# Kernel tuning notes

Hardware: AMD Instinct MI355X
Metric: run time of the kernel (lower is better)

The kernel has to match this reference:

```python
import jax, jax.numpy as jnp
import numpy as np

D = 3            # pseudo-coordinate dimensionality
KS = 5           # kernel size per dim (open B-spline, degree 1)
K = KS ** D      # 125 kernel weight slices
S = 2 ** D       # 8 active linear-basis corners per edge
_COMBOS = np.array([[(s >> d) & 1 for d in range(D)] for s in range(S)], dtype=np.int32)  # [S, D]
_STRIDES = np.array([KS ** (D - 1 - d) for d in range(D)], dtype=np.int32)                # [D]


def spline_basis(pseudo):
    """Degree-1 open B-spline tensor-product basis. pseudo: [E, D] in [0,1].
    Returns basis weights [E, S] and flat kernel indices [E, S]."""
    pos = pseudo * (KS - 1)
    i0 = jnp.clip(jnp.floor(pos), 0, KS - 2).astype(jnp.int32)     # [E, D]
    frac = pos - i0                                                 # [E, D]
    combos = jnp.asarray(_COMBOS)                                   # [S, D]
    basis = jnp.prod(jnp.where(combos[None] == 1, frac[:, None, :], 1.0 - frac[:, None, :]), axis=-1)  # [E, S]
    idx = jnp.sum((i0[:, None, :] + combos[None]) * jnp.asarray(_STRIDES)[None, None, :], axis=-1)      # [E, S]
    return basis, idx


def spline_conv(x, row, col, basis, idx, W, b):
    """out[i] = 1/|N(i)| * sum_{j in N(i)} sum_s b_s(u_ij) * x[j] @ W[k_s] + b.
    x: [N, Fin], W: [K, Fin, Fout]."""
    N = x.shape[0]
    Fout = W.shape[2]
    z = jnp.einsum('ni,kio->nko', x, W).reshape(N * K, Fout)        # [N*K, Fout]
    gathered = z[col[:, None] * K + idx]                            # [E, S, Fout]
    msg = jnp.einsum('es,eso->eo', basis, gathered)                 # [E, Fout]
    out = jax.ops.segment_sum(msg, row, num_segments=N)
    deg = jax.ops.segment_sum(jnp.ones_like(msg[:, 0]), row, num_segments=N)
    return out / jnp.maximum(deg, 1.0)[:, None] + b


def setup_inputs():
    key = jax.random.key(0)
    ks = jax.random.split(key, 13)
    N, E, Fin, Fout = 20000, 320000, 32, 32

    def u(k, shape, size):
        bound = 1.0 / np.sqrt(size)
        return jax.random.uniform(k, shape, jnp.float32, -bound, bound)

    return dict(
        x=jax.random.normal(ks[0], (N, Fin), jnp.float32),
        edge_index=jax.random.randint(ks[1], (2, E), 0, N, dtype=jnp.int32),
        pseudo=jax.random.uniform(ks[2], (E, D), jnp.float32),
        stn1_w=u(ks[3], (K, 1, 64), 1 * S), stn1_b=u(ks[4], (64,), 1 * S),
        stn2_w=u(ks[5], (K, 64, 64), 64 * S), stn2_b=u(ks[6], (64,), 64 * S),
        stn3_w=u(ks[7], (64, 64), 64), stn3_b=u(ks[8], (64,), 64),
        stn4_w=u(ks[9], (64, 3), 64), stn4_b=u(ks[10], (3,), 64),
        conv_w=u(ks[11], (K, Fin, Fout), Fin * S), conv_b=u(ks[12], (Fout,), Fin * S),
    )


def reference(x, edge_index, pseudo, stn1_w, stn1_b, stn2_w, stn2_b,
              stn3_w, stn3_b, stn4_w, stn4_b, conv_w, conv_b):
    N = x.shape[0]
    row, col = edge_index[0], edge_index[1]
    basis, idx = spline_basis(pseudo)
    # local spatial-transformer path: SplineConv(1->64) -> SplineConv(64->64) -> Linear(64->64) -> Linear(64->3)
    h = jnp.ones((N, 1), x.dtype)
    h = jax.nn.elu(spline_conv(h, row, col, basis, idx, stn1_w, stn1_b))
    h = jax.nn.elu(spline_conv(h, row, col, basis, idx, stn2_w, stn2_b))
    h = jax.nn.elu(h @ stn3_w + stn3_b)
    t = h @ stn4_w + stn4_b                                          # [N, 3] per-node pseudo-coord offset
    new_pseudo = jnp.clip(pseudo + t[col] - t[row], 0.0, 1.0)        # transformed pseudo-coordinates
    basis2, idx2 = spline_basis(new_pseudo)
    return spline_conv(x, row, col, basis2, idx2, conv_w, conv_b)
```

## Files before the change

kernel.cpp:

```cpp
#include <hip/hip_runtime.h>
#include <hip/hip_bf16.h>
#include <math.h>


typedef short  s16x8 __attribute__((ext_vector_type(8)));
typedef float  f32x4 __attribute__((ext_vector_type(4)));
typedef _Float16 h16x2 __attribute__((ext_vector_type(2)));

__device__ __forceinline__ unsigned short f2b(float f) {
    __hip_bfloat16 h = __float2bfloat16(f);
    return __builtin_bit_cast(unsigned short, h);
}
__device__ __forceinline__ unsigned short f2h(float f) {
    _Float16 h = (_Float16)f;
    return __builtin_bit_cast(unsigned short, h);
}
__device__ __forceinline__ float h2f(unsigned short u) {
    _Float16 h = __builtin_bit_cast(_Float16, u);
    return (float)h;
}
__device__ __forceinline__ unsigned int fdup(float f) {
    unsigned int h = f2h(f);
    return h | (h << 16);
}
__device__ __forceinline__ h16x2 u2h2(unsigned int u) {
    return __builtin_bit_cast(h16x2, u);
}

__device__ __forceinline__ void spline8(const float u0, const float u1, const float u2,
                                        float* __restrict__ b, int* __restrict__ id) {
    const float u[3] = {u0, u1, u2};
    const int strides[3] = {25, 5, 1};
    float fr[3];
    int   i0[3];
#pragma unroll
    for (int d = 0; d < 3; ++d) {
        float p = u[d] * 4.0f;
        float f = floorf(p);
        f = fminf(fmaxf(f, 0.0f), 3.0f);
        i0[d] = (int)f;
        fr[d] = p - f;
    }
#pragma unroll
    for (int s = 0; s < 8; ++s) {
        float bb = 1.0f;
        int   ii = 0;
#pragma unroll
        for (int d = 0; d < 3; ++d) {
            int c = (s >> d) & 1;
            bb *= c ? fr[d] : (1.0f - fr[d]);
            ii += (i0[d] + c) * strides[d];
        }
        b[s] = bb;
        id[s] = ii;
    }
}

__global__ void hist_kernel(const int* __restrict__ row, const int* __restrict__ col,
                            int* __restrict__ histR, int* __restrict__ histC, int E) {
    int e = blockIdx.x * blockDim.x + threadIdx.x;
    if (e >= E) return;
    atomicAdd(&histR[row[e]], 1);
    atomicAdd(&histC[col[e]], 1);
}

__global__ __launch_bounds__(1024) void scan2_kernel(
        const int* __restrict__ histC, const int* __restrict__ histR,
        int* __restrict__ cstart, int* __restrict__ cursorC,
        int* __restrict__ rowStart, int* __restrict__ cursorR, int N) {
    __shared__ int wsX[16], wsY[16];
    __shared__ int carX, carY;
    int t = threadIdx.x, lane = t & 63, w = t >> 6;
    if (t == 0) { carX = 0; carY = 0; }
    __syncthreads();
    for (int base = 0; base < N; base += 1024) {
        int i = base + t;
        int vx = (i < N) ? histC[i] : 0;
        int vy = (i < N) ? histR[i] : 0;
        int sx = vx, sy = vy;
#pragma unroll
        for (int off = 1; off < 64; off <<= 1) {
            int ux = __shfl_up(sx, off);
            int uy = __shfl_up(sy, off);
            if (lane >= off) { sx += ux; sy += uy; }
        }
        if (lane == 63) { wsX[w] = sx; wsY[w] = sy; }
        __syncthreads();
        if (w == 0 && lane < 16) {
            int ax = wsX[lane], ay = wsY[lane];
#pragma unroll
            for (int off = 1; off < 16; off <<= 1) {
                int ux = __shfl_up(ax, off);
                int uy = __shfl_up(ay, off);
                if (lane >= off) { ax += ux; ay += uy; }
            }
            wsX[lane] = ax; wsY[lane] = ay;
        }
        __syncthreads();
        int wx = (w > 0 ? wsX[w - 1] : 0) + carX;
        int wy = (w > 0 ? wsY[w - 1] : 0) + carY;
        if (i < N) {
            int ex = wx + sx - vx;
            int ey = wy + sy - vy;
            cstart[i] = ex; cursorC[i] = ex;
            rowStart[i] = ey; cursorR[i] = ey;
        }
        __syncthreads();
        if (t == 0) { carX += wsX[15]; carY += wsY[15]; }
        __syncthreads();
    }
}

__global__ void scatterbasis_kernel(
        const int* __restrict__ row, const int* __restrict__ col,
        const float* __restrict__ pseudo,
        int* __restrict__ cursorC, int* __restrict__ cursorR,
        int* __restrict__ jpos, int* __restrict__ colS, int* __restrict__ rs,
        unsigned int* __restrict__ basisH, unsigned char* __restrict__ idxb,
        float* __restrict__ basisR, unsigned char* __restrict__ idxR, int E) {
    int e = blockIdx.x * blockDim.x + threadIdx.x;
    if (e >= E) return;
    int c = col[e], r = row[e];
    int jc = atomicAdd(&cursorC[c], 1);
    int jr = atomicAdd(&cursorR[r], 1);
    jpos[e] = jc;
    colS[jc] = c;
    rs[jc] = jr;
    float b[8]; int id[8];
    spline8(pseudo[e * 3 + 0], pseudo[e * 3 + 1], pseudo[e * 3 + 2], b, id);
#pragma unroll
    for (int s = 0; s < 8; ++s) {
        basisH[(size_t)jc * 8 + s] = fdup(b[s]);
        idxb[(size_t)jc * 8 + s] = (unsigned char)id[s];
        basisR[(size_t)jr * 8 + s] = b[s];
        idxR[(size_t)jr * 8 + s] = (unsigned char)id[s];
    }
}

__global__ void basis1_kernel(const float* __restrict__ pseudo, const int* __restrict__ jpos,
                              float* __restrict__ basis, unsigned char* __restrict__ idxb, int E) {
    int e = blockIdx.x * blockDim.x + threadIdx.x;
    if (e >= E) return;
    float b[8]; int id[8];
    spline8(pseudo[e * 3 + 0], pseudo[e * 3 + 1], pseudo[e * 3 + 2], b, id);
    int j = jpos ? jpos[e] : e;
#pragma unroll
    for (int s = 0; s < 8; ++s) { basis[(size_t)j * 8 + s] = b[s]; idxb[(size_t)j * 8 + s] = (unsigned char)id[s]; }
}

__global__ void basis2h_kernel(const float* __restrict__ pseudo, const float* __restrict__ t,
                               const int* __restrict__ row, const int* __restrict__ col,
                               const int* __restrict__ jpos,
                               unsigned int* __restrict__ basisH,
                               unsigned char* __restrict__ idxb, int E) {
    int e = blockIdx.x * blockDim.x + threadIdx.x;
    if (e >= E) return;
    int r = row[e], c = col[e];
    float u[3];
#pragma unroll
    for (int d = 0; d < 3; ++d) {
        float v = pseudo[e * 3 + d] + t[c * 3 + d] - t[r * 3 + d];
        u[d] = fminf(fmaxf(v, 0.0f), 1.0f);
    }
    float b[8]; int id[8];
    spline8(u[0], u[1], u[2], b, id);
    int j = jpos[e];
#pragma unroll
    for (int s = 0; s < 8; ++s) { basisH[(size_t)j * 8 + s] = fdup(b[s]); idxb[(size_t)j * 8 + s] = (unsigned char)id[s]; }
}

__global__ void basis2_kernel(const float* __restrict__ pseudo, const float* __restrict__ t,
                              const int* __restrict__ row, const int* __restrict__ col,
                              float* __restrict__ basis, unsigned char* __restrict__ idxb, int E) {
    int e = blockIdx.x * blockDim.x + threadIdx.x;
    if (e >= E) return;
    int r = row[e], c = col[e];
    float u[3];
#pragma unroll
    for (int d = 0; d < 3; ++d) {
        float v = pseudo[e * 3 + d] + t[c * 3 + d] - t[r * 3 + d];
        u[d] = fminf(fmaxf(v, 0.0f), 1.0f);
    }
    float b[8]; int id[8];
    spline8(u[0], u[1], u[2], b, id);
#pragma unroll
    for (int s = 0; s < 8; ++s) { basis[(size_t)e * 8 + s] = b[s]; idxb[(size_t)e * 8 + s] = (unsigned char)id[s]; }
}

__global__ void castbf_kernel(const float* __restrict__ in, unsigned short* __restrict__ out,
                              int n) {
    int t = blockIdx.x * blockDim.x + threadIdx.x;
    if (t < n) out[t] = f2b(in[t]);
}

__global__ void pack_w_kernel(const float* __restrict__ W, unsigned short* __restrict__ BF,
                              int Kc, int Fin, int Fout, int ksteps, int CH) {
    int t = blockIdx.x * blockDim.x + threadIdx.x;
    int total = Kc * Fout * Fin;
    if (t >= total) return;
    int c = t / Fin;
    int i = t % Fin;
    int kk = c / Fout, o = c % Fout;
    int split = o / CH;
    int cp = split * (Kc * CH) + kk * CH + (o % CH);
    int ct = cp >> 4, lr = cp & 15;
    int step = i >> 5, rem = i & 31, lg = rem >> 3, jj = rem & 7;
    size_t dst = ((((size_t)ct * ksteps + step) * 4 + lg) * 16 + lr) * 8 + jj;
    BF[dst] = f2b(W[((size_t)kk * Fin + i) * Fout + o]);
}

__global__ __launch_bounds__(256) void phaseB1s_kernel(
        const float* __restrict__ W1, const float* __restrict__ basisR,
        const unsigned char* __restrict__ idxR, const int* __restrict__ rowStart,
        const int* __restrict__ histR, const float* __restrict__ b1,
        unsigned short* __restrict__ h1b, int N) {
    __shared__ float w[125 * 64];
    for (int i = threadIdx.x; i < 125 * 64; i += 256) w[i] = W1[i];
    __syncthreads();
    int n = blockIdx.x * 4 + (threadIdx.x >> 6);
    if (n >= N) return;
    int l = threadIdx.x & 63;
    int s0 = rowStart[n], cnt = histR[n];
    float a = 0.0f;
    for (int i = 0; i < cnt; ++i) {
        const float4* bp = (const float4*)(basisR + (size_t)(s0 + i) * 8);
        float4 b0 = bp[0], b1v = bp[1];
        const uchar4* ip = (const uchar4*)(idxR + (size_t)(s0 + i) * 8);
        uchar4 i0 = ip[0], i1 = ip[1];
        a += b0.x * w[i0.x * 64 + l] + b0.y * w[i0.y * 64 + l]
           + b0.z * w[i0.z * 64 + l] + b0.w * w[i0.w * 64 + l]
           + b1v.x * w[i1.x * 64 + l] + b1v.y * w[i1.y * 64 + l]
           + b1v.z * w[i1.z * 64 + l] + b1v.w * w[i1.w * 64 + l];
    }
    float v = a / fmaxf((float)cnt, 1.0f) + b1[l];
    v = (v > 0.0f) ? v : (expf(v) - 1.0f);
    h1b[(size_t)n * 64 + l] = f2b(v);
}

template<int KSTEPS, int SPLITS, int NODES>
__global__ __launch_bounds__(512) void fusedconv_kernel(
        const unsigned short* __restrict__ A,
        const unsigned short* __restrict__ BF,
        const unsigned int* __restrict__ basisH, const unsigned char* __restrict__ idxb,
        const int* __restrict__ cstart, const int* __restrict__ colS,
        const int* __restrict__ rs,
        unsigned short* __restrict__ msgP, int N, int E) {
    const int ZLD = 2008;
    __shared__ unsigned short ztile[NODES * 2008];
    int n0 = blockIdx.x * NODES;
    if (n0 >= N) return;
    int w = threadIdx.x >> 6, l = threadIdx.x & 63;
    int lr = l & 15, lg = l >> 4;
    const int KD = KSTEPS * 32;
    int arow = n0 + lr; if (arow > N - 1) arow = N - 1;
    s16x8 a[KSTEPS];
#pragma unroll
    for (int st = 0; st < KSTEPS; ++st)
        a[st] = *(const s16x8*)(A + (size_t)arow * KD + st * 32 + lg * 8);
    int estart = cstart[n0];
    int eend = (n0 + NODES < N) ? cstart[n0 + NODES] : E;
    int g = threadIdx.x >> 3, chp = threadIdx.x & 7;
    for (int s = 0; s < SPLITS; ++s) {
        for (int ct = w; ct < 125; ct += 8) {
            f32x4 acc = (f32x4){0.f, 0.f, 0.f, 0.f};
#pragma unroll
            for (int st = 0; st < KSTEPS; ++st) {
                const unsigned short* bp =
                    BF + ((((size_t)(s * 125 + ct) * KSTEPS + st) * 4 + lg) * 16 + lr) * 8;
                s16x8 b = *(const s16x8*)bp;
                acc = __builtin_amdgcn_mfma_f32_16x16x32_bf16(a[st], b, acc, 0, 0, 0);
            }
#pragma unroll
            for (int r = 0; r < 4; ++r) {
                int rl = lg * 4 + r;
                if (rl < NODES)
                    ztile[rl * ZLD + ct * 16 + lr] = f2h(acc[r]);
            }
        }
        __syncthreads();
        unsigned int* mp = (unsigned int*)(msgP + (size_t)s * E * 16);
        for (int j = estart + g; j < eend; j += 64) {
            int node = colS[j] - n0;
            const uint4* bhp = (const uint4*)(basisH + (size_t)j * 8);
            uint4 bA = bhp[0], bB = bhp[1];
            const uchar4* ip = (const uchar4*)(idxb + (size_t)j * 8);
            uchar4 i0 = ip[0], i1 = ip[1];
            const unsigned int* zr = (const unsigned int*)(ztile + node * ZLD);
            unsigned int v0 = zr[i0.x * 8 + chp];
            unsigned int v1 = zr[i0.y * 8 + chp];
            unsigned int v2 = zr[i0.z * 8 + chp];
            unsigned int v3 = zr[i0.w * 8 + chp];
            unsigned int v4 = zr[i1.x * 8 + chp];
            unsigned int v5 = zr[i1.y * 8 + chp];
            unsigned int v6 = zr[i1.z * 8 + chp];
            unsigned int v7 = zr[i1.w * 8 + chp];
            h16x2 ta = u2h2(bA.x) * u2h2(v0);
            ta = u2h2(bA.y) * u2h2(v1) + ta;
            ta = u2h2(bA.z) * u2h2(v2) + ta;
            ta = u2h2(bA.w) * u2h2(v3) + ta;
            h16x2 tb = u2h2(bB.x) * u2h2(v4);
            tb = u2h2(bB.y) * u2h2(v5) + tb;
            tb = u2h2(bB.z) * u2h2(v6) + tb;
            tb = u2h2(bB.w) * u2h2(v7) + tb;
            h16x2 m = ta + tb;
            mp[(size_t)rs[j] * 8 + chp] = __builtin_bit_cast(unsigned int, m);
        }
        __syncthreads();
    }
}

__global__ __launch_bounds__(256) void phaseBs2stn_kernel(
        const unsigned short* __restrict__ msgP, const int* __restrict__ rowStart,
        const int* __restrict__ histR, const float* __restrict__ b2,
        const float* __restrict__ w3, const float* __restrict__ b3,
        const float* __restrict__ w4, const float* __restrict__ b4,
        float* __restrict__ tt, int N, int E) {
    __shared__ float sh[4][64];
    __shared__ float sh3[4][64];
    int wid = threadIdx.x >> 6, l = threadIdx.x & 63;
    int n = blockIdx.x * 4 + wid;
    if (n >= N) return;
    int s0 = rowStart[n], cnt = histR[n];
    const unsigned short* mp = msgP + (size_t)(l >> 4) * E * 16 + (l & 15);
    float a = 0.0f;
    for (int i = 0; i < cnt; ++i)
        a += h2f(mp[(size_t)(s0 + i) * 16]);
    float v = a / fmaxf((float)cnt, 1.0f) + b2[l];
    v = (v > 0.0f) ? v : (expf(v) - 1.0f);
    sh[wid][l] = v;
    __builtin_amdgcn_wave_barrier();
    float v3 = b3[l];
#pragma unroll
    for (int i = 0; i < 64; ++i) v3 += sh[wid][i] * w3[i * 64 + l];
    v3 = (v3 > 0.0f) ? v3 : (expf(v3) - 1.0f);
    sh3[wid][l] = v3;
    __builtin_amdgcn_wave_barrier();
    if (l < 3) {
        float tv = b4[l];
#pragma unroll
        for (int i = 0; i < 64; ++i) tv += sh3[wid][i] * w4[i * 3 + l];
        tt[(size_t)n * 3 + l] = tv;
    }
}

__global__ __launch_bounds__(256) void phaseBs3p_kernel(
        const unsigned short* __restrict__ msgP, const int* __restrict__ rowStart,
        const int* __restrict__ histR, const float* __restrict__ bias,
        float* __restrict__ out, int N, int E) {
    int n = blockIdx.x * 8 + (threadIdx.x >> 5);
    if (n >= N) return;
    int l = threadIdx.x & 31;
    int s0 = rowStart[n], cnt = histR[n];
    const unsigned short* mp = msgP + (size_t)(l >> 4) * E * 16 + (l & 15);
    float a = 0.0f;
    for (int i = 0; i < cnt; ++i)
        a += h2f(mp[(size_t)(s0 + i) * 16]);
    out[(size_t)n * 32 + l] = a / fmaxf((float)cnt, 1.0f) + bias[l];
}

__global__ __launch_bounds__(64) void stn34_kernel(
        const float* __restrict__ h2, const float* __restrict__ w3,
        const float* __restrict__ b3, const float* __restrict__ w4,
        const float* __restrict__ b4, float* __restrict__ t, int N) {
    int n = blockIdx.x;
    int o = threadIdx.x;
    __shared__ float sh[64];
    __shared__ float sh3[64];
    sh[o] = h2[n * 64 + o];
    __syncthreads();
    float v = b3[o];
#pragma unroll
    for (int i = 0; i < 64; ++i) v += sh[i] * w3[i * 64 + o];
    v = (v > 0.0f) ? v : (expf(v) - 1.0f);
    sh3[o] = v;
    __syncthreads();
    if (o < 3) {
        float tv = b4[o];
#pragma unroll
        for (int i = 0; i < 64; ++i) tv += sh3[i] * w4[i * 3 + o];
        t[n * 3 + o] = tv;
    }
}

__global__ __launch_bounds__(256) void conv1_at_kernel(
        const float* __restrict__ basis, const unsigned char* __restrict__ idxb,
        const int* __restrict__ row, const float* __restrict__ W1,
        float* __restrict__ acc, int E) {
    int j = blockIdx.x * 4 + (threadIdx.x >> 6);
    if (j >= E) return;
    int l = threadIdx.x & 63;
    float m = 0.0f;
#pragma unroll
    for (int s = 0; s < 8; ++s) m += basis[(size_t)j * 8 + s] * W1[idxb[(size_t)j * 8 + s] * 64 + l];
    atomicAdd(&acc[(size_t)row[j] * 64 + l], m);
}

__global__ __launch_bounds__(256) void conv2f_kernel(
        const float* __restrict__ h1, const float* __restrict__ basis,
        const unsigned char* __restrict__ idxb, const int* __restrict__ row,
        const int* __restrict__ col, const float* __restrict__ W2,
        float* __restrict__ acc, int E) {
    int wid = threadIdx.x >> 6;
    int lane = threadIdx.x & 63;
    int e = blockIdx.x * 4 + wid;
    __shared__ float sh[4][64];
    bool active = (e < E);
    int c = active ? col[e] : 0;
    if (active) sh[wid][lane] = h1[(size_t)c * 64 + lane];
    __syncthreads();
    if (!active) return;
    float m = 0.0f;
#pragma unroll
    for (int s = 0; s < 8; ++s) {
        const float* Wk = W2 + (size_t)idxb[(size_t)e * 8 + s] * 4096;
        float ms = 0.0f;
#pragma unroll
        for (int i = 0; i < 64; ++i) ms += sh[wid][i] * Wk[i * 64 + lane];
        m += basis[(size_t)e * 8 + s] * ms;
    }
    atomicAdd(&acc[(size_t)row[e] * 64 + lane], m);
}

__global__ __launch_bounds__(256) void conv3f_kernel(
        const float* __restrict__ x, const float* __restrict__ basis,
        const unsigned char* __restrict__ idxb, const int* __restrict__ row,
        const int* __restrict__ col, const float* __restrict__ Wc,
        float* __restrict__ acc, int E) {
    int wid = threadIdx.x >> 6;
    int lane = threadIdx.x & 63;
    int e = blockIdx.x * 4 + wid;
    __shared__ float sx[4][32];
    bool active = (e < E);
    int c = active ? col[e] : 0;
    if (active && lane < 32) sx[wid][lane] = x[(size_t)c * 32 + lane];
    __syncthreads();
    int half = lane >> 5;
    int o = lane & 31;
    float m = 0.0f;
    if (active) {
#pragma unroll
        for (int s2 = 0; s2 < 4; ++s2) {
            int s = half * 4 + s2;
            const float* Wk = Wc + (size_t)idxb[(size_t)e * 8 + s] * 1024;
            float ms = 0.0f;
#pragma unroll
            for (int i = 0; i < 32; ++i) ms += sx[wid][i] * Wk[i * 32 + o];
            m += basis[(size_t)e * 8 + s] * ms;
        }
    }
    m += __shfl_xor(m, 32);
    if (active && lane < 32) atomicAdd(&acc[(size_t)row[e] * 32 + o], m);
}

__global__ void finalize_kernel(const float* __restrict__ acc, const int* __restrict__ histR,
                                const float* __restrict__ bias, float* __restrict__ outF,
                                unsigned short* __restrict__ outB,
                                int N, int F, int do_elu) {
    int t = blockIdx.x * blockDim.x + threadIdx.x;
    if (t >= N * F) return;
    int n = t / F, o = t % F;
    float v = acc[t] / fmaxf((float)histR[n], 1.0f) + bias[o];
    if (do_elu) v = (v > 0.0f) ? v : (expf(v) - 1.0f);
    if (outF) outF[t] = v;
    if (outB) outB[t] = f2b(v);
}

extern "C" void kernel_launch(void* const* d_in, const int* in_sizes, int n_in,
                              void* d_out, int out_size, void* d_ws, size_t ws_size,
                              hipStream_t stream) {
    const float* x      = (const float*)d_in[0];
    const int*   ei     = (const int*)d_in[1];
    const float* pseudo = (const float*)d_in[2];
    const float* w1     = (const float*)d_in[3];
    const float* b1     = (const float*)d_in[4];
    const float* w2     = (const float*)d_in[5];
    const float* b2     = (const float*)d_in[6];
    const float* w3     = (const float*)d_in[7];
    const float* b3     = (const float*)d_in[8];
    const float* w4     = (const float*)d_in[9];
    const float* b4     = (const float*)d_in[10];
    const float* wc     = (const float*)d_in[11];
    const float* cb     = (const float*)d_in[12];
    float* out = (float*)d_out;

    const int N = in_sizes[0] / 32;
    const int E = in_sizes[1] / 2;
    const int* row = ei;
    const int* col = ei + E;
    const int KC = 125;
    const int NODES = 12;

    char* p = (char*)d_ws;
    int* histR = (int*)p; p += (size_t)N * sizeof(int);
    int* histC = (int*)p; p += (size_t)N * sizeof(int);
    size_t zero_bytes = (size_t)(p - (char*)d_ws);
    int* cstart   = (int*)p; p += (size_t)N * sizeof(int);
    int* cursorC  = (int*)p; p += (size_t)N * sizeof(int);
    int* rowStart = (int*)p; p += (size_t)N * sizeof(int);
    int* cursorR  = (int*)p; p += (size_t)N * sizeof(int);
    int* jpos = (int*)p; p += (size_t)E * sizeof(int);
    int* colS = (int*)p; p += (size_t)E * sizeof(int);
    int* rs   = (int*)p; p += (size_t)E * sizeof(int);
    float* tt = (float*)p; p += (size_t)N * 3 * sizeof(float);
    unsigned int* basisH = (unsigned int*)p;
    float* basisF = (float*)p; p += (size_t)E * 8 * sizeof(float);
    unsigned char* idxb = (unsigned char*)p; p += (size_t)E * 8;
    unsigned short* h1b = (unsigned short*)p; p += (size_t)N * 64 * sizeof(short);
    unsigned short* xb  = (unsigned short*)p; p += (size_t)N * 32 * sizeof(short);
    unsigned short* BF2 = (unsigned short*)p; p += (size_t)KC * 64 * 64 * sizeof(short);
    unsigned short* BF3 = (unsigned short*)p; p += (size_t)KC * 32 * 32 * sizeof(short);
    unsigned short* msg = (unsigned short*)p; p += (size_t)E * 64 * sizeof(short);
    float* basisR = (float*)p; p += (size_t)E * 8 * sizeof(float);
    unsigned char* idxR = (unsigned char*)p; p += (size_t)E * 8;
    size_t fixed = (size_t)(p - (char*)d_ws);
    bool fast = ws_size >= fixed;

    hipMemsetAsync(d_ws, 0, zero_bytes, stream);
    hist_kernel<<<(E + 255) / 256, 256, 0, stream>>>(row, col, histR, histC, E);

    if (fast) {
        pack_w_kernel<<<(KC * 64 * 64 + 255) / 256, 256, 0, stream>>>(w2, BF2, KC, 64, 64, 2, 16);
        pack_w_kernel<<<(KC * 32 * 32 + 255) / 256, 256, 0, stream>>>(wc, BF3, KC, 32, 32, 1, 16);
        castbf_kernel<<<(N * 32 + 255) / 256, 256, 0, stream>>>(x, xb, N * 32);

        scan2_kernel<<<1, 1024, 0, stream>>>(histC, histR, cstart, cursorC, rowStart, cursorR, N);
        scatterbasis_kernel<<<(E + 255) / 256, 256, 0, stream>>>(
            row, col, pseudo, cursorC, cursorR, jpos, colS, rs, basisH, idxb, basisR, idxR, E);

        phaseB1s_kernel<<<(N + 3) / 4, 256, 0, stream>>>(w1, basisR, idxR, rowStart,
                                                         histR, b1, h1b, N);
        const int NB = (N + NODES - 1) / NODES;
        fusedconv_kernel<2, 4, 12><<<NB, 512, 0, stream>>>(
            h1b, BF2, basisH, idxb, cstart, colS, rs, msg, N, E);
        phaseBs2stn_kernel<<<(N + 3) / 4, 256, 0, stream>>>(msg, rowStart, histR, b2,
                                                            w3, b3, w4, b4, tt, N, E);
        basis2h_kernel<<<(E + 255) / 256, 256, 0, stream>>>(pseudo, tt, row, col, jpos,
                                                            basisH, idxb, E);
        fusedconv_kernel<1, 2, 12><<<NB, 512, 0, stream>>>(
            xb, BF3, basisH, idxb, cstart, colS, rs, msg, N, E);
        phaseBs3p_kernel<<<(N + 7) / 8, 256, 0, stream>>>(msg, rowStart, histR, cb, out, N, E);
    } else {
        float* acc1 = (float*)msg;
        float* acc2 = acc1 + (size_t)N * 64;
        float* acc3 = acc2 + (size_t)N * 64;
        float* h1f  = acc3 + (size_t)N * 32;
        float* h2f_ = h1f  + (size_t)N * 64;
        size_t acc_bytes = (size_t)N * (64 + 64 + 32) * sizeof(float);
        hipMemsetAsync((void*)acc1, 0, acc_bytes, stream);

        basis1_kernel<<<(E + 255) / 256, 256, 0, stream>>>(pseudo, nullptr, basisF, idxb, E);
        conv1_at_kernel<<<(E + 3) / 4, 256, 0, stream>>>(basisF, idxb, row, w1, acc1, E);
        finalize_kernel<<<(N * 64 + 255) / 256, 256, 0, stream>>>(acc1, histR, b1, h1f, nullptr, N, 64, 1);
        conv2f_kernel<<<(E + 3) / 4, 256, 0, stream>>>(h1f, basisF, idxb, row, col, w2, acc2, E);
        finalize_kernel<<<(N * 64 + 255) / 256, 256, 0, stream>>>(acc2, histR, b2, h2f_, nullptr, N, 64, 1);
        stn34_kernel<<<N, 64, 0, stream>>>(h2f_, w3, b3, w4, b4, tt, N);
        basis2_kernel<<<(E + 255) / 256, 256, 0, stream>>>(pseudo, tt, row, col, basisF, idxb, E);
        conv3f_kernel<<<(E + 3) / 4, 256, 0, stream>>>(x, basisF, idxb, row, col, wc, acc3, E);
        finalize_kernel<<<(N * 32 + 255) / 256, 256, 0, stream>>>(acc3, histR, cb, out, nullptr, N, 32, 0);
    }
}
```

Before: 376.3 us.

## Replace first spline conv with per-node basis histogram and MFMA GEMM

Because the first conv's input is all ones, its output per node depends only on the per-node sum of basis weights over the 125 kernel slots. The scatter kernel now accumulates those sums with float atomics into a zeroed N×128 buffer, and a small MFMA kernel multiplies that buffer by the packed W1 and applies degree normalization, bias and ELU. This removes the row-sorted basis/index arrays and the per-edge gather loop in shared memory. In exchange it adds 2.56M float atomics, a 10MB memset, and bf16 rounding of the accumulated coefficients.

```diff
diff --git a/kernel.cpp b/kernel.cpp
--- a/kernel.cpp
+++ b/kernel.cpp
@@ -117,7 +117,7 @@
         int* __restrict__ cursorC, int* __restrict__ cursorR,
         int* __restrict__ jpos, int* __restrict__ colS, int* __restrict__ rs,
         unsigned int* __restrict__ basisH, unsigned char* __restrict__ idxb,
-        float* __restrict__ basisR, unsigned char* __restrict__ idxR, int E) {
+        float* __restrict__ Cacc, int E) {
     int e = blockIdx.x * blockDim.x + threadIdx.x;
     if (e >= E) return;
     int c = col[e], r = row[e];
@@ -128,12 +128,12 @@
     rs[jc] = jr;
     float b[8]; int id[8];
     spline8(pseudo[e * 3 + 0], pseudo[e * 3 + 1], pseudo[e * 3 + 2], b, id);
+    float* crow = Cacc + (size_t)r * 128;
 #pragma unroll
     for (int s = 0; s < 8; ++s) {
         basisH[(size_t)jc * 8 + s] = fdup(b[s]);
         idxb[(size_t)jc * 8 + s] = (unsigned char)id[s];
-        basisR[(size_t)jr * 8 + s] = b[s];
-        idxR[(size_t)jr * 8 + s] = (unsigned char)id[s];
+        atomicAdd(&crow[id[s]], b[s]);
     }
 }
 
@@ -209,32 +209,59 @@
     BF[dst] = f2b(W[((size_t)kk * Fin + i) * Fout + o]);
 }
 
-__global__ __launch_bounds__(256) void phaseB1s_kernel(
-        const float* __restrict__ W1, const float* __restrict__ basisR,
-        const unsigned char* __restrict__ idxR, const int* __restrict__ rowStart,
+__global__ void pack_w1_kernel(const float* __restrict__ W1, unsigned short* __restrict__ BF1) {
+    int t = blockIdx.x * blockDim.x + threadIdx.x;
+    if (t >= 128 * 64) return;
+    int c = t >> 7;
+    int i = t & 127;
+    int ct = c >> 4, lr = c & 15;
+    int step = i >> 5, rem = i & 31, lg = rem >> 3, jj = rem & 7;
+    size_t dst = (((size_t)(ct * 4 + step) * 4 + lg) * 16 + lr) * 8 + jj;
+    BF1[dst] = (i < 125) ? f2b(W1[i * 64 + c]) : (unsigned short)0;
+}
+
+__global__ __launch_bounds__(256) void zgemm1_kernel(
+        const float* __restrict__ C, const unsigned short* __restrict__ BF1,
         const int* __restrict__ histR, const float* __restrict__ b1,
-        unsigned short* __restrict__ h1b, int N) {
-    __shared__ float w[125 * 64];
-    for (int i = threadIdx.x; i < 125 * 64; i += 256) w[i] = W1[i];
-    __syncthreads();
-    int n = blockIdx.x * 4 + (threadIdx.x >> 6);
-    if (n >= N) return;
-    int l = threadIdx.x & 63;
-    int s0 = rowStart[n], cnt = histR[n];
-    float a = 0.0f;
-    for (int i = 0; i < cnt; ++i) {
-        const float4* bp = (const float4*)(basisR + (size_t)(s0 + i) * 8);
-        float4 b0 = bp[0], b1v = bp[1];
-        const uchar4* ip = (const uchar4*)(idxR + (size_t)(s0 + i) * 8);
-        uchar4 i0 = ip[0], i1 = ip[1];
-        a += b0.x * w[i0.x * 64 + l] + b0.y * w[i0.y * 64 + l]
-           + b0.z * w[i0.z * 64 + l] + b0.w * w[i0.w * 64 + l]
-           + b1v.x * w[i1.x * 64 + l] + b1v.y * w[i1.y * 64 + l]
-           + b1v.z * w[i1.z * 64 + l] + b1v.w * w[i1.w * 64 + l];
-    }
-    float v = a / fmaxf((float)cnt, 1.0f) + b1[l];
-    v = (v > 0.0f) ? v : (expf(v) - 1.0f);
-    h1b[(size_t)n * 64 + l] = f2b(v);
+        unsigned short* __restrict__ h1b, int M) {
+    int w = threadIdx.x >> 6, l = threadIdx.x & 63;
+    int lr = l & 15, lg = l >> 4;
+    int m0 = blockIdx.x * 64 + w * 16;
+    f32x4 acc[4];
+#pragma unroll
+    for (int cf = 0; cf < 4; ++cf) acc[cf] = (f32x4){0.f, 0.f, 0.f, 0.f};
+    int arow = m0 + lr; if (arow > M - 1) arow = M - 1;
+    const float* crow = C + (size_t)arow * 128;
+#pragma unroll
+    for (int step = 0; step < 4; ++step) {
+        float4 fa = *(const float4*)(crow + step * 32 + lg * 8);
+        float4 fb = *(const float4*)(crow + step * 32 + lg * 8 + 4);
+        s16x8 a;
+        a[0] = (short)f2b(fa.x); a[1] = (short)f2b(fa.y);
+        a[2] = (short)f2b(fa.z); a[3] = (short)f2b(fa.w);
+        a[4] = (short)f2b(fb.x); a[5] = (short)f2b(fb.y);
+        a[6] = (short)f2b(fb.z); a[7] = (short)f2b(fb.w);
+#pragma unroll
+        for (int cf = 0; cf < 4; ++cf) {
+            const unsigned short* bp =
+                BF1 + (((size_t)(cf * 4 + step) * 4 + lg) * 16 + lr) * 8;
+            s16x8 b = *(const s16x8*)bp;
+            acc[cf] = __builtin_amdgcn_mfma_f32_16x16x32_bf16(a, b, acc[cf], 0, 0, 0);
+        }
+    }
+#pragma unroll
+    for (int cf = 0; cf < 4; ++cf) {
+        int colc = cf * 16 + lr;
+#pragma unroll
+        for (int r = 0; r < 4; ++r) {
+            int rowc = m0 + lg * 4 + r;
+            if (rowc < M) {
+                float v = acc[cf][r] / fmaxf((float)histR[rowc], 1.0f) + b1[colc];
+                v = (v > 0.0f) ? v : (expf(v) - 1.0f);
+                h1b[(size_t)rowc * 64 + colc] = f2b(v);
+            }
+        }
+    }
 }
 
 template<int KSTEPS, int SPLITS, int NODES>
@@ -493,6 +520,7 @@
     char* p = (char*)d_ws;
     int* histR = (int*)p; p += (size_t)N * sizeof(int);
     int* histC = (int*)p; p += (size_t)N * sizeof(int);
+    float* Cacc = (float*)p; p += (size_t)N * 128 * sizeof(float);
     size_t zero_bytes = (size_t)(p - (char*)d_ws);
     int* cstart   = (int*)p; p += (size_t)N * sizeof(int);
     int* cursorC  = (int*)p; p += (size_t)N * sizeof(int);
@@ -509,9 +537,8 @@
     unsigned short* xb  = (unsigned short*)p; p += (size_t)N * 32 * sizeof(short);
     unsigned short* BF2 = (unsigned short*)p; p += (size_t)KC * 64 * 64 * sizeof(short);
     unsigned short* BF3 = (unsigned short*)p; p += (size_t)KC * 32 * 32 * sizeof(short);
+    unsigned short* BF1 = (unsigned short*)p; p += (size_t)128 * 64 * sizeof(short);
     unsigned short* msg = (unsigned short*)p; p += (size_t)E * 64 * sizeof(short);
-    float* basisR = (float*)p; p += (size_t)E * 8 * sizeof(float);
-    unsigned char* idxR = (unsigned char*)p; p += (size_t)E * 8;
     size_t fixed = (size_t)(p - (char*)d_ws);
     bool fast = ws_size >= fixed;
 
@@ -521,14 +548,15 @@
     if (fast) {
         pack_w_kernel<<<(KC * 64 * 64 + 255) / 256, 256, 0, stream>>>(w2, BF2, KC, 64, 64, 2, 16);
         pack_w_kernel<<<(KC * 32 * 32 + 255) / 256, 256, 0, stream>>>(wc, BF3, KC, 32, 32, 1, 16);
+        pack_w1_kernel<<<(128 * 64 + 255) / 256, 256, 0, stream>>>(w1, BF1);
         castbf_kernel<<<(N * 32 + 255) / 256, 256, 0, stream>>>(x, xb, N * 32);
 
         scan2_kernel<<<1, 1024, 0, stream>>>(histC, histR, cstart, cursorC, rowStart, cursorR, N);
         scatterbasis_kernel<<<(E + 255) / 256, 256, 0, stream>>>(
-            row, col, pseudo, cursorC, cursorR, jpos, colS, rs, basisH, idxb, basisR, idxR, E);
-
-        phaseB1s_kernel<<<(N + 3) / 4, 256, 0, stream>>>(w1, basisR, idxR, rowStart,
-                                                         histR, b1, h1b, N);
+            row, col, pseudo, cursorC, cursorR, jpos, colS, rs, basisH, idxb, Cacc, E);
+
+        zgemm1_kernel<<<(N + 63) / 64, 256, 0, stream>>>(Cacc, BF1, histR, b1, h1b, N);
+
         const int NB = (N + NODES - 1) / NODES;
         fusedconv_kernel<2, 4, 12><<<NB, 512, 0, stream>>>(
             h1b, BF2, basisH, idxb, cstart, colS, rs, msg, N, E);
```

Result: slower. 462.9 us (+23.0%).
